# Kernel tuning notes

Hardware: AMD Instinct MI355X
Metric: run time of the kernel (lower is better)

## Reference

```python
import jax, jax.numpy as jnp
import numpy as np


def _2div(arr):
    arr_res = arr.copy()
    arr_pieces = []
    pa = 0
    st = 0
    needdivcnt = 0
    for i, a in enumerate(arr):
        if a != pa:
            arr_pieces.append([st, i])
            if i - st != 1:
                needdivcnt += 1
            pa = a
            st = i
    arr_pieces.append([st, len(arr)])
    if len(arr) - st != 1:
        needdivcnt += 1
    offset = range(len(arr_pieces), len(arr_pieces) + needdivcnt)
    p = 0
    for arr_p in arr_pieces:
        length = arr_p[1] - arr_p[0]
        if length == 1:
            continue
        half_len = int(np.ceil(length / 2))
        for j in range(arr_p[0] + half_len, arr_p[1]):
            arr_res[j] = offset[p]
        p += 1
    return arr_res


def get_division_tree(n_agents):
    agent2divitreeindex = np.arange(n_agents)
    np.random.shuffle(agent2divitreeindex)
    max_div = np.ceil(np.log2(n_agents)).astype(int)
    levels = np.zeros(shape=(max_div + 1, n_agents), dtype=int)
    for ith in range(1, len(levels)):
        levels[ith, :] = _2div(levels[ith - 1, :])
    res_levels = levels.copy()
    for i, idx in enumerate(agent2divitreeindex):
        res_levels[:, i] = levels[:, idx]
    return res_levels


def setup_inputs() -> dict:
    B, A, H, NACT = 2048, 50, 512, 64
    F = H + A  # in-features of first Linear (hidden + one-hot agent id)
    np.random.seed(0)
    div_tree = get_division_tree(A)
    routing = jnp.asarray(div_tree[-1], dtype=jnp.int32)  # max_level routing: agent -> net index
    key = jax.random.key(0)
    k0, k1, k2 = jax.random.split(key, 3)
    x_in = jax.random.normal(k0, (B, A, H), dtype=jnp.float32)
    # stacked per-net parameters (n_nets == n_agent independent 2-layer MLPs)
    W1 = jax.random.normal(k1, (A, F, H), dtype=jnp.float32) * (1.0 / np.sqrt(F))
    b1 = jnp.zeros((A, H), dtype=jnp.float32)
    W2 = jax.random.normal(k2, (A, H, NACT), dtype=jnp.float32) * (1.0 / np.sqrt(H))
    b2 = jnp.zeros((A, NACT), dtype=jnp.float32)
    return {"x_in": x_in, "W1": W1, "b1": b1, "W2": W2, "b2": b2, "routing": routing}


def reference(x_in, W1, b1, W2, b2, routing):
    # x_in: [B, A, H]; routing: [A] int (which net each agent uses)
    B, A, H = x_in.shape
    # add_onehot_id_at_last_dim: append agent-id one-hot -> [B, A, H+A]
    onehot = jnp.broadcast_to(jnp.eye(A, dtype=x_in.dtype), (B, A, A))
    x0 = jnp.concatenate([x_in, onehot], axis=-1)
    # gather routed expert weights per agent
    W1r, b1r = W1[routing], b1[routing]   # [A, H+A, H], [A, H]
    W2r, b2r = W2[routing], b2[routing]   # [A, H, NACT], [A, NACT]
    h = jax.nn.relu(jnp.einsum('baf,afh->bah', x0, W1r) + b1r)
    out = jnp.einsum('bah,ahn->ban', h, W2r) + b2r  # [B, A, NACT]
    return out
```

## Files before the change

### kernel.cpp

```cpp
#include <hip/hip_runtime.h>

typedef __attribute__((ext_vector_type(8))) short bf16x8;
typedef __attribute__((ext_vector_type(4))) float f32x4;
typedef __attribute__((ext_vector_type(4))) unsigned short u16x4;
typedef __attribute__((ext_vector_type(8))) unsigned short u16x8;

#define B_ 2048
#define A_ 50
#define H_ 512
#define NACT_ 64
#define F_ 562
#define BM_ 64
#define BK_ 32
#define NSTEP_ (H_ / BK_)

#define WS_W1T 0
#define WS_W2T ((size_t)A_ * H_ * H_ * 2)
#define WS_B1 (WS_W2T + (size_t)A_ * NACT_ * H_ * 2)
#define WS_B2 (WS_B1 + (size_t)A_ * H_ * 4)

static __device__ __forceinline__ unsigned short f2bf(float f) {
  unsigned int u = __builtin_bit_cast(unsigned int, f);
  u += 0x7fffu + ((u >> 16) & 1u);
  return (unsigned short)(u >> 16);
}

static __device__ __forceinline__ void gld_lds16(const unsigned short* src,
                                                 unsigned short* dst) {
  __builtin_amdgcn_global_load_lds(
      (const __attribute__((address_space(1))) unsigned int*)(const void*)src,
      (__attribute__((address_space(3))) unsigned int*)(void*)dst, 16, 0, 0);
}

static __device__ __forceinline__ int clamp_r(int r) {
  return r < 0 ? 0 : (r > A_ - 1 ? A_ - 1 : r);
}

__global__ void prep_w1(const float* __restrict__ w1,
                        const int* __restrict__ routing,
                        unsigned short* __restrict__ w1t) {
  const int bid = blockIdx.x;
  const int a = bid / 64;
  const int tile = bid - a * 64;
  const int tk = tile & 7, tj = tile >> 3;
  const int k0 = tk * 64, j0 = tj * 64;
  const int r = clamp_r(routing[a]);
  __shared__ float tl[64][65];
  const int t = threadIdx.x;
  const int c = t & 63, q = t >> 6;
#pragma unroll
  for (int i = 0; i < 16; ++i) {
    const int kl = q + i * 4;
    tl[kl][c] = w1[((size_t)r * F_ + k0 + kl) * H_ + j0 + c];
  }
  __syncthreads();
#pragma unroll
  for (int it = 0; it < 2; ++it) {
    const int jl = t >> 2, c2 = t & 3;
    const int kc = it * 4 + (c2 ^ (jl & 3));
    u16x8 v;
#pragma unroll
    for (int e = 0; e < 8; ++e) v[e] = f2bf(tl[kc * 8 + e][jl]);
    unsigned short* dst = w1t +
        (((size_t)a * 16 + tk * 2 + it) * H_ + j0 + jl) * 32 + c2 * 8;
    *(u16x8*)dst = v;
  }
}

__global__ void prep_w2(const float* __restrict__ w2,
                        const int* __restrict__ routing,
                        unsigned short* __restrict__ w2t) {
  const int bid = blockIdx.x;
  const int a = bid >> 3;
  const int tk = bid & 7;
  const int k0 = tk * 64;
  const int r = clamp_r(routing[a]);
  __shared__ float tl[64][65];
  const int t = threadIdx.x;
  const int c = t & 63, q = t >> 6;
#pragma unroll
  for (int i = 0; i < 16; ++i) {
    const int kl = q + i * 4;
    tl[kl][c] = w2[((size_t)r * H_ + k0 + kl) * NACT_ + c];
  }
  __syncthreads();
#pragma unroll
  for (int i = 0; i < 16; ++i) {
    const int nl = q + i * 4;
    w2t[((size_t)a * NACT_ + nl) * H_ + k0 + c] = f2bf(tl[c][nl]);
  }
}

__global__ void prep_bias(const float* __restrict__ w1,
                          const float* __restrict__ b1,
                          const float* __restrict__ b2,
                          const int* __restrict__ routing,
                          float* __restrict__ bias1, float* __restrict__ bias2) {
  const int a = blockIdx.x;
  const int t = threadIdx.x;
  const int r = clamp_r(routing[a]);
  bias1[a * H_ + t] = b1[(size_t)r * H_ + t] + w1[((size_t)r * F_ + H_ + a) * H_ + t];
  if (t < NACT_) bias2[a * NACT_ + t] = b2[r * NACT_ + t];
}

__global__ __launch_bounds__(512, 4) void divtree_main(
    const float* __restrict__ x, const unsigned short* __restrict__ w1t,
    const unsigned short* __restrict__ w2t, const float* __restrict__ bias1,
    const float* __restrict__ bias2, float* __restrict__ out) {
  __shared__ union {
    struct {
      unsigned short w1[2][H_ * BK_];
      unsigned short xs[2][BM_ * BK_];
    } st;
    unsigned short h[BM_ * H_];
    float outb[BM_][66];
  } sm;

  const int bid = blockIdx.x;
  const int swz = (bid & 7) * 200 + (bid >> 3);
  const int a = swz >> 5;
  const int mblk = swz & 31;
  const int b0 = mblk * BM_;

  const int tid = threadIdx.x;
  const int lane = tid & 63;
  const int w = tid >> 6;
  const int l16 = lane & 15;
  const int lk = lane >> 4;
  const int sxor = lk ^ (l16 & 3);

  const int wj = w * 64;

  const unsigned short* w1ta = w1t + (size_t)a * (H_ * H_);

  const int xrow = tid >> 3;
  const int xq = tid & 7;
  const float* xbase =
      x + ((size_t)(b0 + xrow) * A_ + (size_t)a) * H_ + (size_t)xq * 4;
  const int xs_off = xrow * BK_ + ((xq >> 1) ^ (xrow & 3)) * 8 + (xq & 1) * 4;

  const int afr_base = (wj + l16) * BK_ + sxor * 8;
  const int bfr_base = l16 * BK_ + sxor * 8;

  f32x4 acc[4][4];
#pragma unroll
  for (int i = 0; i < 4; ++i)
#pragma unroll
    for (int j = 0; j < 4; ++j) acc[i][j] = (f32x4){0.f, 0.f, 0.f, 0.f};

  f32x4 xr[3];

  {
    const f32x4 xv0 = *(const f32x4*)xbase;
#pragma unroll
    for (int i = 0; i < 4; ++i)
      gld_lds16(w1ta + ((size_t)(i * 512 + tid) << 3),
                sm.st.w1[0] + (size_t)(i * 512 + (w << 6)) * 8);
    xr[1] = *(const f32x4*)(xbase + 1 * BK_);
    xr[2] = *(const f32x4*)(xbase + 2 * BK_);
    u16x4 v;
#pragma unroll
    for (int e = 0; e < 4; ++e) v[e] = f2bf(xv0[e]);
    *(u16x4*)(sm.st.xs[0] + xs_off) = v;
  }

#pragma unroll
  for (int t = 0; t < NSTEP_; ++t) {
    const int buf = t & 1;
    if (t <= NSTEP_ - 3)
      asm volatile("s_waitcnt vmcnt(1) lgkmcnt(0)" ::: "memory");
    else
      asm volatile("s_waitcnt vmcnt(0) lgkmcnt(0)" ::: "memory");
    __builtin_amdgcn_sched_barrier(0);
    __builtin_amdgcn_s_barrier();
    __builtin_amdgcn_sched_barrier(0);
    if (t + 1 < NSTEP_) {
      const unsigned short* wsrc = w1ta + (size_t)(t + 1) * (H_ * BK_);
      unsigned short* wdst = sm.st.w1[buf ^ 1];
#pragma unroll
      for (int i = 0; i < 4; ++i)
        gld_lds16(wsrc + ((size_t)(i * 512 + tid) << 3),
                  wdst + (size_t)(i * 512 + (w << 6)) * 8);
    }
    if (t + 3 < NSTEP_)
      xr[(t + 3) % 3] = *(const f32x4*)(xbase + (size_t)(t + 3) * BK_);
    const unsigned short* w1s = sm.st.w1[buf];
    const unsigned short* xss = sm.st.xs[buf];
    bf16x8 bfr[4];
#pragma unroll
    for (int mf = 0; mf < 4; ++mf)
      bfr[mf] = *(const bf16x8*)(xss + bfr_base + mf * (16 * BK_));
    __builtin_amdgcn_s_setprio(1);
#pragma unroll
    for (int jf = 0; jf < 4; ++jf) {
      const bf16x8 afr = *(const bf16x8*)(w1s + afr_base + jf * (16 * BK_));
#pragma unroll
      for (int mf = 0; mf < 4; ++mf)
        acc[jf][mf] = __builtin_amdgcn_mfma_f32_16x16x32_bf16(
            afr, bfr[mf], acc[jf][mf], 0, 0, 0);
    }
    __builtin_amdgcn_s_setprio(0);
    if (t + 1 < NSTEP_) {
      const f32x4 xv = xr[(t + 1) % 3];
      u16x4 v;
#pragma unroll
      for (int e = 0; e < 4; ++e) v[e] = f2bf(xv[e]);
      *(u16x4*)(sm.st.xs[buf ^ 1] + xs_off) = v;
    }
  }
  __syncthreads();

  const float* b1p = bias1 + a * H_;
#pragma unroll
  for (int jf = 0; jf < 4; ++jf) {
    const f32x4 bv = *(const f32x4*)(b1p + wj + jf * 16 + lk * 4);
    const int cbase = (wj >> 3) + jf * 2 + (lk >> 1);
    const int half4 = (lk & 1) * 4;
#pragma unroll
    for (int mf = 0; mf < 4; ++mf) {
      u16x4 hv;
#pragma unroll
      for (int r = 0; r < 4; ++r) {
        float f = acc[jf][mf][r] + bv[r];
        f = f > 0.f ? f : 0.f;
        hv[r] = f2bf(f);
      }
      const int m = mf * 16 + l16;
      const int off = m * H_ + ((cbase ^ (l16 & 7))) * 8 + half4;
      *(u16x4*)(sm.h + off) = hv;
    }
  }
  __syncthreads();

  const int m0 = (w & 1) * 32;
  const int n0 = (w >> 1) * 16;
  const unsigned short* w2p =
      w2t + ((size_t)a * NACT_ + n0 + l16) * H_ + lk * 8;
  f32x4 acc2[2];
  acc2[0] = (f32x4){0.f, 0.f, 0.f, 0.f};
  acc2[1] = (f32x4){0.f, 0.f, 0.f, 0.f};
#pragma unroll
  for (int kf = 0; kf < 16; ++kf) {
    const bf16x8 bf2 = *(const bf16x8*)(w2p + kf * 32);
#pragma unroll
    for (int mf = 0; mf < 2; ++mf) {
      const int row = m0 + mf * 16 + l16;
      const int off = row * H_ + (((kf * 4 + lk) ^ (l16 & 7))) * 8;
      const bf16x8 af2 = *(const bf16x8*)(sm.h + off);
      acc2[mf] = __builtin_amdgcn_mfma_f32_16x16x32_bf16(af2, bf2, acc2[mf],
                                                         0, 0, 0);
    }
  }
  const float b2v = bias2[a * NACT_ + n0 + l16];
  __syncthreads();
#pragma unroll
  for (int mf = 0; mf < 2; ++mf)
#pragma unroll
    for (int r = 0; r < 4; ++r)
      sm.outb[m0 + mf * 16 + lk * 4 + r][n0 + l16] = acc2[mf][r] + b2v;
  __syncthreads();

  {
    const int row = tid >> 3;
    const int q8 = (tid & 7) * 8;
    const f32x4 v0 = *(const f32x4*)(&sm.outb[row][q8]);
    const f32x4 v1 = *(const f32x4*)(&sm.outb[row][q8 + 4]);
    float* op = out + ((size_t)(b0 + row) * A_ + a) * NACT_ + q8;
    *(f32x4*)op = v0;
    *(f32x4*)(op + 4) = v1;
  }
}

extern "C" void kernel_launch(void* const* d_in, const int* in_sizes, int n_in,
                              void* d_out, int out_size, void* d_ws,
                              size_t ws_size, hipStream_t stream) {
  const float* x = (const float*)d_in[0];
  const float* w1 = (const float*)d_in[1];
  const float* b1 = (const float*)d_in[2];
  const float* w2 = (const float*)d_in[3];
  const float* b2 = (const float*)d_in[4];
  const int* routing = (const int*)d_in[5];
  float* out = (float*)d_out;

  char* ws = (char*)d_ws;
  unsigned short* w1t = (unsigned short*)(ws + WS_W1T);
  unsigned short* w2t = (unsigned short*)(ws + WS_W2T);
  float* bias1 = (float*)(ws + WS_B1);
  float* bias2 = (float*)(ws + WS_B2);

  prep_w1<<<A_ * 64, 256, 0, stream>>>(w1, routing, w1t);
  prep_w2<<<A_ * 8, 256, 0, stream>>>(w2, routing, w2t);
  prep_bias<<<A_, 512, 0, stream>>>(w1, b1, b2, routing, bias1, bias2);
  divtree_main<<<A_ * (B_ / BM_), 512, 0, stream>>>(x, w1t, w2t, bias1, bias2,
                                                    out);
}
```

Before: 143.2 us.

## Stage full x tile in LDS once and stream W1 fragments directly into registers

The first GEMM no longer double-buffers W1 and x slices through LDS with global_load_lds and per-step barriers. The whole 64x512 bf16 x tile is converted and stored into swizzled LDS up front, and each wave loads its W1 fragments straight from global into registers, ping-ponging two register sets. This removes the per-step block barrier and the W1 LDS traffic, but each wave re-reads W1 from global or L2 without sharing. It also raises register pressure, and the launch-bounds occupancy hint is dropped.

```diff
diff --git a/kernel.cpp b/kernel.cpp
--- a/kernel.cpp
+++ b/kernel.cpp
@@ -12,7 +12,7 @@
 #define F_ 562
 #define BM_ 64
 #define BK_ 32
-#define NSTEP_ (H_ / BK_)
+#define NSTEP_ 16
 
 #define WS_W1T 0
 #define WS_W2T ((size_t)A_ * H_ * H_ * 2)
@@ -23,13 +23,6 @@
   unsigned int u = __builtin_bit_cast(unsigned int, f);
   u += 0x7fffu + ((u >> 16) & 1u);
   return (unsigned short)(u >> 16);
-}
-
-static __device__ __forceinline__ void gld_lds16(const unsigned short* src,
-                                                 unsigned short* dst) {
-  __builtin_amdgcn_global_load_lds(
-      (const __attribute__((address_space(1))) unsigned int*)(const void*)src,
-      (__attribute__((address_space(3))) unsigned int*)(void*)dst, 16, 0, 0);
 }
 
 static __device__ __forceinline__ int clamp_r(int r) {
@@ -54,10 +47,10 @@
     tl[kl][c] = w1[((size_t)r * F_ + k0 + kl) * H_ + j0 + c];
   }
   __syncthreads();
+  const int jl = t >> 2, c2 = t & 3;
 #pragma unroll
   for (int it = 0; it < 2; ++it) {
-    const int jl = t >> 2, c2 = t & 3;
-    const int kc = it * 4 + (c2 ^ (jl & 3));
+    const int kc = it * 4 + c2;
     u16x8 v;
 #pragma unroll
     for (int e = 0; e < 8; ++e) v[e] = f2bf(tl[kc * 8 + e][jl]);
@@ -103,15 +96,12 @@
   if (t < NACT_) bias2[a * NACT_ + t] = b2[r * NACT_ + t];
 }
 
-__global__ __launch_bounds__(512, 4) void divtree_main(
+__global__ __launch_bounds__(512) void divtree_v13(
     const float* __restrict__ x, const unsigned short* __restrict__ w1t,
     const unsigned short* __restrict__ w2t, const float* __restrict__ bias1,
     const float* __restrict__ bias2, float* __restrict__ out) {
   __shared__ union {
-    struct {
-      unsigned short w1[2][H_ * BK_];
-      unsigned short xs[2][BM_ * BK_];
-    } st;
+    unsigned short xs[BM_ * H_];
     unsigned short h[BM_ * H_];
     float outb[BM_][66];
   } sm;
@@ -127,20 +117,35 @@
   const int w = tid >> 6;
   const int l16 = lane & 15;
   const int lk = lane >> 4;
-  const int sxor = lk ^ (l16 & 3);
-
+  const int l7 = l16 & 7;
   const int wj = w * 64;
 
   const unsigned short* w1ta = w1t + (size_t)a * (H_ * H_);
 
-  const int xrow = tid >> 3;
-  const int xq = tid & 7;
-  const float* xbase =
-      x + ((size_t)(b0 + xrow) * A_ + (size_t)a) * H_ + (size_t)xq * 4;
-  const int xs_off = xrow * BK_ + ((xq >> 1) ^ (xrow & 3)) * 8 + (xq & 1) * 4;
-
-  const int afr_base = (wj + l16) * BK_ + sxor * 8;
-  const int bfr_base = l16 * BK_ + sxor * 8;
+  {
+    const int xm = tid >> 3;
+    const int xq = tid & 7;
+    const float* xrowp =
+        x + ((size_t)(b0 + xm) * A_ + (size_t)a) * H_ + (size_t)xq * 64;
+    f32x4 xv[16];
+#pragma unroll
+    for (int i = 0; i < 16; ++i) xv[i] = *(const f32x4*)(xrowp + i * 4);
+#pragma unroll
+    for (int j = 0; j < 8; ++j) {
+      u16x8 v;
+#pragma unroll
+      for (int e = 0; e < 4; ++e) {
+        v[e] = f2bf(xv[2 * j][e]);
+        v[4 + e] = f2bf(xv[2 * j + 1][e]);
+      }
+      const int c = xq * 8 + j;
+      *(u16x8*)(sm.xs + xm * H_ + (c ^ (xm & 7)) * 8) = v;
+    }
+  }
+  __syncthreads();
+
+  const unsigned short* wfr =
+      w1ta + (size_t)(wj + l16) * 32 + (size_t)(lk * 8);
 
   f32x4 acc[4][4];
 #pragma unroll
@@ -148,65 +153,41 @@
 #pragma unroll
     for (int j = 0; j < 4; ++j) acc[i][j] = (f32x4){0.f, 0.f, 0.f, 0.f};
 
-  f32x4 xr[3];
-
-  {
-    const f32x4 xv0 = *(const f32x4*)xbase;
-#pragma unroll
-    for (int i = 0; i < 4; ++i)
-      gld_lds16(w1ta + ((size_t)(i * 512 + tid) << 3),
-                sm.st.w1[0] + (size_t)(i * 512 + (w << 6)) * 8);
-    xr[1] = *(const f32x4*)(xbase + 1 * BK_);
-    xr[2] = *(const f32x4*)(xbase + 2 * BK_);
-    u16x4 v;
-#pragma unroll
-    for (int e = 0; e < 4; ++e) v[e] = f2bf(xv0[e]);
-    *(u16x4*)(sm.st.xs[0] + xs_off) = v;
-  }
+  bf16x8 wrA[4], wrB[4];
+
+#pragma unroll
+  for (int jf = 0; jf < 4; ++jf)
+    wrA[jf] = *(const bf16x8*)(wfr + jf * (16 * 32));
 
 #pragma unroll
   for (int t = 0; t < NSTEP_; ++t) {
-    const int buf = t & 1;
-    if (t <= NSTEP_ - 3)
-      asm volatile("s_waitcnt vmcnt(1) lgkmcnt(0)" ::: "memory");
-    else
-      asm volatile("s_waitcnt vmcnt(0) lgkmcnt(0)" ::: "memory");
-    __builtin_amdgcn_sched_barrier(0);
-    __builtin_amdgcn_s_barrier();
-    __builtin_amdgcn_sched_barrier(0);
     if (t + 1 < NSTEP_) {
-      const unsigned short* wsrc = w1ta + (size_t)(t + 1) * (H_ * BK_);
-      unsigned short* wdst = sm.st.w1[buf ^ 1];
-#pragma unroll
-      for (int i = 0; i < 4; ++i)
-        gld_lds16(wsrc + ((size_t)(i * 512 + tid) << 3),
-                  wdst + (size_t)(i * 512 + (w << 6)) * 8);
-    }
-    if (t + 3 < NSTEP_)
-      xr[(t + 3) % 3] = *(const f32x4*)(xbase + (size_t)(t + 3) * BK_);
-    const unsigned short* w1s = sm.st.w1[buf];
-    const unsigned short* xss = sm.st.xs[buf];
+      const unsigned short* p = wfr + (size_t)(t + 1) * (H_ * BK_);
+      if (t & 1) {
+#pragma unroll
+        for (int jf = 0; jf < 4; ++jf)
+          wrA[jf] = *(const bf16x8*)(p + jf * (16 * 32));
+      } else {
+#pragma unroll
+        for (int jf = 0; jf < 4; ++jf)
+          wrB[jf] = *(const bf16x8*)(p + jf * (16 * 32));
+      }
+    }
+    const int post = ((t * 4 + lk) ^ l7) * 8;
     bf16x8 bfr[4];
 #pragma unroll
     for (int mf = 0; mf < 4; ++mf)
-      bfr[mf] = *(const bf16x8*)(xss + bfr_base + mf * (16 * BK_));
+      bfr[mf] = *(const bf16x8*)(sm.xs + (mf * 16 + l16) * H_ + post);
     __builtin_amdgcn_s_setprio(1);
 #pragma unroll
     for (int jf = 0; jf < 4; ++jf) {
-      const bf16x8 afr = *(const bf16x8*)(w1s + afr_base + jf * (16 * BK_));
+      const bf16x8 afr = (t & 1) ? wrB[jf] : wrA[jf];
 #pragma unroll
       for (int mf = 0; mf < 4; ++mf)
         acc[jf][mf] = __builtin_amdgcn_mfma_f32_16x16x32_bf16(
             afr, bfr[mf], acc[jf][mf], 0, 0, 0);
     }
     __builtin_amdgcn_s_setprio(0);
-    if (t + 1 < NSTEP_) {
-      const f32x4 xv = xr[(t + 1) % 3];
-      u16x4 v;
-#pragma unroll
-      for (int e = 0; e < 4; ++e) v[e] = f2bf(xv[e]);
-      *(u16x4*)(sm.st.xs[buf ^ 1] + xs_off) = v;
-    }
   }
   __syncthreads();
 
@@ -291,6 +272,6 @@
   prep_w1<<<A_ * 64, 256, 0, stream>>>(w1, routing, w1t);
   prep_w2<<<A_ * 8, 256, 0, stream>>>(w2, routing, w2t);
   prep_bias<<<A_, 512, 0, stream>>>(w1, b1, b2, routing, bias1, bias2);
-  divtree_main<<<A_ * (B_ / BM_), 512, 0, stream>>>(x, w1t, w2t, bias1, bias2,
-                                                    out);
-}
+  divtree_v13<<<A_ * (B_ / BM_), 512, 0, stream>>>(x, w1t, w2t, bias1, bias2,
+                                                   out);
+}
```

Measured after the change: 165.1 us. 15.3% more time.
